# Kernel optimization log

Measured on AMD Instinct MI355X. Metric: run time of the kernel, lower is better.

## Reference

```python
import jax, jax.numpy as jnp
import numpy as np

B, N, L, D = 4, 128, 20, 512


def setup_inputs() -> dict:
    key = jax.random.key(0)
    ks = jax.random.split(key, 8)
    return {
        "f_b": jax.random.normal(ks[0], (B, N, D), jnp.float32),
        "f_w": jax.random.normal(ks[1], (B, L, D), jnp.float32),
        "f_s": jax.random.normal(ks[2], (B, D), jnp.float32),
        "f_m": jax.random.normal(ks[3], (B, N, N, D), jnp.float32),
        "Wq": jax.random.normal(ks[4], (D, D), jnp.float32) / np.sqrt(D).astype(np.float32),
        "bq": jax.random.normal(ks[5], (D,), jnp.float32) * 0.02,
        "Wk": jax.random.normal(ks[6], (D, D), jnp.float32) / np.sqrt(D).astype(np.float32),
        "bk": jax.random.normal(ks[7], (D,), jnp.float32) * 0.02,
    }


def reference(f_b, f_w, f_s, f_m, Wq, bq, Wk, bk):
    d = f_b.shape[-1]
    scale = jnp.asarray(1.0 / np.sqrt(d), f_b.dtype)
    # cross-attention: boundary features attend to word features
    q = f_b @ Wq.T + bq                                   # [B,N,D]
    k = f_w @ Wk.T + bk                                   # [B,L,D]
    attn = jax.nn.softmax(jnp.einsum('bnd,bld->bnl', q, k) * scale, axis=-1)
    f_baq = jnp.einsum('bnl,bld->bnd', attn, f_w)         # [B,N,D]
    # sentence-gated boundary features
    f_bq = f_b * (f_baq + f_s[:, None, :])                # [B,N,D]
    # boundary self-attention
    A_b = jax.nn.softmax(jnp.einsum('bnd,bmd->bnm', f_bq, f_bq) * scale, axis=-1)
    f_bb = jnp.einsum('bnm,bmd->bnd', A_b, f_b)           # [B,N,D]
    # gated moment-map reduction: sum_i A_b[b,i,j] * sigmoid(f_m*f_s)*f_m
    g_m = jax.nn.sigmoid(f_m * f_s[:, None, None, :])     # [B,N,N,D]
    f_bm = jnp.einsum('bij,bijd->bjd', A_b, g_m * f_m)    # [B,N,D]
    return f_bb + f_b + f_bm
```

## Files before the change

### kernel.cpp

```cpp
#include <hip/hip_runtime.h>
#include <hip/hip_bf16.h>

#define Bc 4
#define Nc 128
#define Lc 20
#define Dc 512
#define SCALE 0.04419417382415922f
#define NL2E -1.4426950408889634f

#if __has_builtin(__builtin_amdgcn_exp2f)
#define EXP2(x) __builtin_amdgcn_exp2f(x)
#else
#define EXP2(x) __expf((x) * 0.6931471805599453f)
#endif

typedef float vf4 __attribute__((ext_vector_type(4)));

#if __has_builtin(__builtin_nontemporal_load)
#define NT_LOAD4(p) __builtin_nontemporal_load((const vf4*)(p))
#else
#define NT_LOAD4(p) (*(const vf4*)(p))
#endif

__global__ __launch_bounds__(256)
void proj_gemm(const float* __restrict__ f_b, const float* __restrict__ f_w,
               const float* __restrict__ Wq, const float* __restrict__ bq,
               const float* __restrict__ Wk, const float* __restrict__ bk,
               float* __restrict__ qb, float* __restrict__ kb) {
    const int t  = threadIdx.x;
    const int tc = blockIdx.x, ty = blockIdx.y, kz = blockIdx.z;
    const bool isq = ty < 8;
    if (!isq && kz >= 4) return;
    const int c0    = tc * 64;
    const int r0    = isq ? ty * 64 : (ty - 8) * 64;
    const int nrows = isq ? 512 : 80;
    const int KB    = isq ? 64 : 128;
    const int kbase = isq ? kz * 64 : kz * 128;
    const float* Ain  = isq ? f_b : f_w;
    const float* W    = isq ? Wq : Wk;
    const float* bias = isq ? bq : bk;
    float* C          = isq ? (qb + kz * 512 * Dc) : (kb + kz * 80 * Dc);

    __shared__ __align__(16) float As[16][68];
    __shared__ __align__(16) float Bs[16][68];

    const int srow = t >> 2;
    const int sk4  = (t & 3) * 4;
    const int arow = min(r0 + srow, nrows - 1);
    const int wrow = c0 + srow;

    const int rr = (t >> 4) * 4;
    const int cc = (t & 15) * 4;
    float acc[4][4] = {};

    const float* Aptr = Ain + arow * Dc + kbase + sk4;
    const float* Wptr = W   + wrow * Dc + kbase + sk4;
    float4 ga = *(const float4*)Aptr;
    float4 gb = *(const float4*)Wptr;

    for (int kk0 = 16; kk0 <= KB; kk0 += 16) {
        __syncthreads();
        As[sk4 + 0][srow] = ga.x; As[sk4 + 1][srow] = ga.y;
        As[sk4 + 2][srow] = ga.z; As[sk4 + 3][srow] = ga.w;
        Bs[sk4 + 0][srow] = gb.x; Bs[sk4 + 1][srow] = gb.y;
        Bs[sk4 + 2][srow] = gb.z; Bs[sk4 + 3][srow] = gb.w;
        __syncthreads();
        if (kk0 < KB) {
            ga = *(const float4*)(Aptr + kk0);
            gb = *(const float4*)(Wptr + kk0);
        }
#pragma unroll
        for (int kk = 0; kk < 16; kk++) {
            const float4 av = *(const float4*)&As[kk][rr];
            const float4 bv = *(const float4*)&Bs[kk][cc];
            acc[0][0] = fmaf(av.x, bv.x, acc[0][0]);
            acc[0][1] = fmaf(av.x, bv.y, acc[0][1]);
            acc[0][2] = fmaf(av.x, bv.z, acc[0][2]);
            acc[0][3] = fmaf(av.x, bv.w, acc[0][3]);
            acc[1][0] = fmaf(av.y, bv.x, acc[1][0]);
            acc[1][1] = fmaf(av.y, bv.y, acc[1][1]);
            acc[1][2] = fmaf(av.y, bv.z, acc[1][2]);
            acc[1][3] = fmaf(av.y, bv.w, acc[1][3]);
            acc[2][0] = fmaf(av.z, bv.x, acc[2][0]);
            acc[2][1] = fmaf(av.z, bv.y, acc[2][1]);
            acc[2][2] = fmaf(av.z, bv.z, acc[2][2]);
            acc[2][3] = fmaf(av.z, bv.w, acc[2][3]);
            acc[3][0] = fmaf(av.w, bv.x, acc[3][0]);
            acc[3][1] = fmaf(av.w, bv.y, acc[3][1]);
            acc[3][2] = fmaf(av.w, bv.z, acc[3][2]);
            acc[3][3] = fmaf(av.w, bv.w, acc[3][3]);
        }
    }

    float4 bv4 = make_float4(0.f, 0.f, 0.f, 0.f);
    if (kz == 0) bv4 = *(const float4*)&bias[c0 + cc];
#pragma unroll
    for (int i = 0; i < 4; i++) {
        const int orow = r0 + rr + i;
        if (orow < nrows) {
            float4 o;
            o.x = acc[i][0] + bv4.x; o.y = acc[i][1] + bv4.y;
            o.z = acc[i][2] + bv4.z; o.w = acc[i][3] + bv4.w;
            *(float4*)&C[orow * Dc + c0 + cc] = o;
        }
    }
}

__global__ __launch_bounds__(256)
void cross_attn_gate(const float* __restrict__ qb, const float* __restrict__ kb,
                     const float* __restrict__ f_w, const float* __restrict__ f_b,
                     const float* __restrict__ f_s, float* __restrict__ f_bq) {
    const int bn = blockIdx.x;
    const int b  = bn >> 7;
    const int t  = threadIdx.x;
    const int lane = t & 63, wave = t >> 6;

    __shared__ __align__(16) float qs[Dc];
    __shared__ float sc[32];
    __shared__ float invs;

    {
        float2 s = make_float2(0.f, 0.f);
#pragma unroll
        for (int h = 0; h < 8; h++) {
            const float2 u = ((const float2*)(qb + h * 512 * Dc + bn * Dc))[t];
            s.x += u.x; s.y += u.y;
        }
        ((float2*)qs)[t] = s;
    }
    __syncthreads();

    const float4* q4 = (const float4*)qs;
    const float4 qa = q4[lane];
    const float4 qv = q4[lane + 64];

    for (int l = wave; l < Lc; l += 4) {
        float4 ka = make_float4(0.f, 0.f, 0.f, 0.f);
        float4 kv = make_float4(0.f, 0.f, 0.f, 0.f);
#pragma unroll
        for (int h = 0; h < 4; h++) {
            const float4* kr = (const float4*)(kb + h * 80 * Dc + (b * Lc + l) * Dc);
            const float4 u = kr[lane];
            const float4 v = kr[lane + 64];
            ka.x += u.x; ka.y += u.y; ka.z += u.z; ka.w += u.w;
            kv.x += v.x; kv.y += v.y; kv.z += v.z; kv.w += v.w;
        }
        float s = qa.x * ka.x + qa.y * ka.y + qa.z * ka.z + qa.w * ka.w
                + qv.x * kv.x + qv.y * kv.y + qv.z * kv.z + qv.w * kv.w;
#pragma unroll
        for (int d = 32; d >= 1; d >>= 1) s += __shfl_down(s, d, 64);
        if (lane == 0) sc[l] = s * SCALE;
    }
    __syncthreads();

    if (t == 0) {
        float mx = sc[0];
        for (int l = 1; l < Lc; l++) mx = fmaxf(mx, sc[l]);
        float sum = 0.f;
        for (int l = 0; l < Lc; l++) { float e = __expf(sc[l] - mx); sc[l] = e; sum += e; }
        invs = 1.0f / sum;
    }
    __syncthreads();
    const float inv = invs;

    const float2* fw2 = (const float2*)(f_w + b * Lc * Dc);
    float2 acc = make_float2(0.f, 0.f);
#pragma unroll 5
    for (int l = 0; l < Lc; l++) {
        const float2 v = fw2[l * 256 + t];
        const float w = sc[l];
        acc.x = fmaf(w, v.x, acc.x);
        acc.y = fmaf(w, v.y, acc.y);
    }
    const float2 s2 = ((const float2*)(f_s + b * Dc))[t];
    const float2 fb2 = ((const float2*)(f_b + bn * Dc))[t];
    float2 o;
    o.x = fb2.x * (acc.x * inv + s2.x);
    o.y = fb2.y * (acc.y * inv + s2.y);
    ((float2*)(f_bq + bn * Dc))[t] = o;
}

__global__ __launch_bounds__(512)
void self_attn_scores(const float* __restrict__ f_bq,
                      float* __restrict__ A_b, float* __restrict__ A_bT) {
    const int bn = blockIdx.x;
    const int b  = bn >> 7, n = bn & 127;
    const int t  = threadIdx.x;
    const int lane = t & 63, wave = t >> 6;

    __shared__ __align__(16) float qrow[Dc];
    __shared__ float sc[Nc];
    __shared__ float redm[2];
    __shared__ float reds[2];

    qrow[t] = f_bq[bn * Dc + t];
    __syncthreads();

    const float4* q4 = (const float4*)qrow;
    const float4 qa = q4[lane];
    const float4 qv = q4[lane + 64];

    for (int m = wave; m < Nc; m += 8) {
        const float4* kr = (const float4*)(f_bq + (b * Nc + m) * Dc);
        const float4 va = kr[lane];
        const float4 vb = kr[lane + 64];
        float s = qa.x * va.x + qa.y * va.y + qa.z * va.z + qa.w * va.w
                + qv.x * vb.x + qv.y * vb.y + qv.z * vb.z + qv.w * vb.w;
#pragma unroll
        for (int d = 32; d >= 1; d >>= 1) s += __shfl_down(s, d, 64);
        if (lane == 0) sc[m] = s * SCALE;
    }
    __syncthreads();

    float sval = 0.f, e = 0.f;
    if (t < Nc) {
        sval = sc[t];
        float m = sval;
#pragma unroll
        for (int d = 32; d >= 1; d >>= 1) m = fmaxf(m, __shfl_xor(m, d, 64));
        if (lane == 0) redm[wave] = m;
    }
    __syncthreads();
    if (t < Nc) {
        const float mx = fmaxf(redm[0], redm[1]);
        e = __expf(sval - mx);
        float s = e;
#pragma unroll
        for (int d = 32; d >= 1; d >>= 1) s += __shfl_xor(s, d, 64);
        if (lane == 0) reds[wave] = s;
    }
    __syncthreads();
    if (t < Nc) {
        const float a = e * (1.0f / (reds[0] + reds[1]));
        A_b[bn * Nc + t] = a;
        A_bT[(b * Nc + t) * Nc + n] = a;
    }
}

__global__ __launch_bounds__(256, 4)
void moment_final(const float* __restrict__ f_m, const float* __restrict__ f_s,
                  const float* __restrict__ A_b, const float* __restrict__ A_bT,
                  const float* __restrict__ f_b, float* __restrict__ out) {
    const int bj = blockIdx.x;
    const int b  = bj >> 7, j = bj & 127;
    const int dh = blockIdx.y;
    const int t  = threadIdx.x;
    const int c  = t & 63;
    const int g  = t >> 6;

    __shared__ float w[Nc];
    __shared__ float ar[Nc];
    __shared__ __align__(16) float4 pex[3][64];

    if (t < Nc) w[t] = A_bT[bj * Nc + t];
    else        ar[t - Nc] = A_b[bj * Nc + (t - Nc)];
    __syncthreads();

    const int c4 = dh * 64 + c;
    const float4 s4 = ((const float4*)(f_s + b * Dc))[c4];
    const float4 ns = make_float4(NL2E * s4.x, NL2E * s4.y, NL2E * s4.z, NL2E * s4.w);

    float4 acc = make_float4(0.f, 0.f, 0.f, 0.f);
    const float* fm = f_m;
    const long istride = (long)Nc * Dc;
    long idx = ((long)(b * Nc + g * 32) * Nc + j) * Dc + c4 * 4;

#pragma unroll 1
    for (int ii = 0; ii < 32; ii += 8) {
        vf4 mv[8];
#pragma unroll
        for (int u = 0; u < 8; u++)
            mv[u] = NT_LOAD4(fm + idx + (long)u * istride);
        idx += 8 * istride;
#pragma unroll
        for (int u = 0; u < 8; u++) {
            const float ww = w[g * 32 + ii + u];
            const vf4 m4 = mv[u];
            acc.x = fmaf(ww * m4.x, __builtin_amdgcn_rcpf(1.f + EXP2(m4.x * ns.x)), acc.x);
            acc.y = fmaf(ww * m4.y, __builtin_amdgcn_rcpf(1.f + EXP2(m4.y * ns.y)), acc.y);
            acc.z = fmaf(ww * m4.z, __builtin_amdgcn_rcpf(1.f + EXP2(m4.z * ns.z)), acc.z);
            acc.w = fmaf(ww * m4.w, __builtin_amdgcn_rcpf(1.f + EXP2(m4.w * ns.w)), acc.w);
        }
    }

    const float4* fb4 = (const float4*)(f_b + b * Nc * Dc);
    const int mbase = g * 32;
#pragma unroll 4
    for (int m = mbase; m < mbase + 32; m++) {
        const float a = ar[m];
        const float4 v = fb4[m * (Dc / 4) + c4];
        acc.x = fmaf(a, v.x, acc.x); acc.y = fmaf(a, v.y, acc.y);
        acc.z = fmaf(a, v.z, acc.z); acc.w = fmaf(a, v.w, acc.w);
    }

    if (g != 0) pex[g - 1][c] = acc;
    __syncthreads();
    if (g == 0) {
#pragma unroll
        for (int p = 0; p < 3; p++) {
            const float4 q = pex[p][c];
            acc.x += q.x; acc.y += q.y; acc.z += q.z; acc.w += q.w;
        }
        const float4 r = fb4[j * (Dc / 4) + c4];
        acc.x += r.x; acc.y += r.y; acc.z += r.z; acc.w += r.w;
        ((float4*)out)[bj * (Dc / 4) + c4] = acc;
    }
}

extern "C" void kernel_launch(void* const* d_in, const int* in_sizes, int n_in,
                              void* d_out, int out_size, void* d_ws, size_t ws_size,
                              hipStream_t stream) {
    const float* f_b = (const float*)d_in[0];
    const float* f_w = (const float*)d_in[1];
    const float* f_s = (const float*)d_in[2];
    const float* f_m = (const float*)d_in[3];
    const float* Wq  = (const float*)d_in[4];
    const float* bq  = (const float*)d_in[5];
    const float* Wk  = (const float*)d_in[6];
    const float* bk  = (const float*)d_in[7];
    float* out = (float*)d_out;

    float* ws   = (float*)d_ws;
    float* qb   = ws;
    float* kb   = qb   + 8 * 512 * Dc;
    float* f_bq = kb   + 4 * 80 * Dc;
    float* A_b  = f_bq + 512 * Dc;
    float* A_bT = A_b  + 512 * Nc;

    proj_gemm<<<dim3(8, 10, 8), 256, 0, stream>>>(f_b, f_w, Wq, bq, Wk, bk, qb, kb);
    cross_attn_gate<<<Bc * Nc, 256, 0, stream>>>(qb, kb, f_w, f_b, f_s, f_bq);
    self_attn_scores<<<Bc * Nc, 512, 0, stream>>>(f_bq, A_b, A_bT);
    moment_final<<<dim3(Bc * Nc, 2), 256, 0, stream>>>(f_m, f_s, A_b, A_bT, f_b, out);
}
```

Baseline: 234.1 us.

## Prefetch f_m into cache via extra blocks in earlier kernels

Adds extra blocks to the projection, cross-attention and self-attention kernels that only load slices of the large f_m tensor and discard the values, so the data sits in cache (likely the large last-level cache) before the moment reduction kernel runs. The moment kernel switches from nontemporal loads to normal cached loads so it can hit those lines. The aim is to overlap reading the dominant f_m traffic with the small earlier kernels. The risk is that f_m (128 MB) is larger than the cache, so most of it will be evicted and the extra reads add DRAM traffic.

```diff
diff --git a/kernel.cpp b/kernel.cpp
--- a/kernel.cpp
+++ b/kernel.cpp
@@ -14,25 +14,34 @@
 #define EXP2(x) __expf((x) * 0.6931471805599453f)
 #endif
 
-typedef float vf4 __attribute__((ext_vector_type(4)));
-
-#if __has_builtin(__builtin_nontemporal_load)
-#define NT_LOAD4(p) __builtin_nontemporal_load((const vf4*)(p))
-#else
-#define NT_LOAD4(p) (*(const vf4*)(p))
-#endif
+
+__device__ __forceinline__ void prefetch_fm(const float4* p, int iters, int stride) {
+    for (int it = 0; it < iters; ++it) {
+        const float4 v = p[it * stride];
+        asm volatile("" :: "v"(v.x), "v"(v.y), "v"(v.z), "v"(v.w));
+    }
+}
 
 __global__ __launch_bounds__(256)
 void proj_gemm(const float* __restrict__ f_b, const float* __restrict__ f_w,
                const float* __restrict__ Wq, const float* __restrict__ bq,
                const float* __restrict__ Wk, const float* __restrict__ bk,
+               const float* __restrict__ f_m,
                float* __restrict__ qb, float* __restrict__ kb) {
-    const int t  = threadIdx.x;
-    const int tc = blockIdx.x, ty = blockIdx.y, kz = blockIdx.z;
-    const bool isq = ty < 8;
-    if (!isq && kz >= 4) return;
+    const int bid = blockIdx.x;
+    const int t   = threadIdx.x;
+
+    if (bid >= 576) {
+        prefetch_fm((const float4*)f_m + (long)(bid - 576) * 4096 + t, 16, 256);
+        return;
+    }
+
+    const bool isq = bid < 512;
+    int tc, ty, kz;
+    if (isq) { kz = bid >> 6; ty = (bid >> 3) & 7; tc = bid & 7; }
+    else     { const int x = bid - 512; kz = x >> 4; ty = (x >> 3) & 1; tc = x & 7; }
     const int c0    = tc * 64;
-    const int r0    = isq ? ty * 64 : (ty - 8) * 64;
+    const int r0    = ty * 64;
     const int nrows = isq ? 512 : 80;
     const int KB    = isq ? 64 : 128;
     const int kbase = isq ? kz * 64 : kz * 128;
@@ -109,10 +118,18 @@
 __global__ __launch_bounds__(256)
 void cross_attn_gate(const float* __restrict__ qb, const float* __restrict__ kb,
                      const float* __restrict__ f_w, const float* __restrict__ f_b,
-                     const float* __restrict__ f_s, float* __restrict__ f_bq) {
-    const int bn = blockIdx.x;
+                     const float* __restrict__ f_s, const float* __restrict__ f_m,
+                     float* __restrict__ f_bq) {
+    const int bid = blockIdx.x;
+    const int t  = threadIdx.x;
+
+    if (bid >= 512) {
+        prefetch_fm((const float4*)f_m + 1835008L + (long)(bid - 512) * 4096 + t, 16, 256);
+        return;
+    }
+
+    const int bn = bid;
     const int b  = bn >> 7;
-    const int t  = threadIdx.x;
     const int lane = t & 63, wave = t >> 6;
 
     __shared__ __align__(16) float qs[Dc];
@@ -181,11 +198,18 @@
 }
 
 __global__ __launch_bounds__(512)
-void self_attn_scores(const float* __restrict__ f_bq,
+void self_attn_scores(const float* __restrict__ f_bq, const float* __restrict__ f_m,
                       float* __restrict__ A_b, float* __restrict__ A_bT) {
-    const int bn = blockIdx.x;
+    const int bid = blockIdx.x;
+    const int t  = threadIdx.x;
+
+    if (bid >= 512) {
+        prefetch_fm((const float4*)f_m + 3932160L + (long)(bid - 512) * 5120 + t, 10, 512);
+        return;
+    }
+
+    const int bn = bid;
     const int b  = bn >> 7, n = bn & 127;
-    const int t  = threadIdx.x;
     const int lane = t & 63, wave = t >> 6;
 
     __shared__ __align__(16) float qrow[Dc];
@@ -261,21 +285,21 @@
     const float4 ns = make_float4(NL2E * s4.x, NL2E * s4.y, NL2E * s4.z, NL2E * s4.w);
 
     float4 acc = make_float4(0.f, 0.f, 0.f, 0.f);
-    const float* fm = f_m;
-    const long istride = (long)Nc * Dc;
-    long idx = ((long)(b * Nc + g * 32) * Nc + j) * Dc + c4 * 4;
+    const float4* fm4 = (const float4*)f_m;
+    const long istride = (long)Nc * (Dc / 4);
+    long idx = ((long)(b * Nc + g * 32) * Nc + j) * (Dc / 4) + c4;
 
 #pragma unroll 1
     for (int ii = 0; ii < 32; ii += 8) {
-        vf4 mv[8];
+        float4 mv[8];
 #pragma unroll
         for (int u = 0; u < 8; u++)
-            mv[u] = NT_LOAD4(fm + idx + (long)u * istride);
+            mv[u] = fm4[idx + (long)u * istride];
         idx += 8 * istride;
 #pragma unroll
         for (int u = 0; u < 8; u++) {
             const float ww = w[g * 32 + ii + u];
-            const vf4 m4 = mv[u];
+            const float4 m4 = mv[u];
             acc.x = fmaf(ww * m4.x, __builtin_amdgcn_rcpf(1.f + EXP2(m4.x * ns.x)), acc.x);
             acc.y = fmaf(ww * m4.y, __builtin_amdgcn_rcpf(1.f + EXP2(m4.y * ns.y)), acc.y);
             acc.z = fmaf(ww * m4.z, __builtin_amdgcn_rcpf(1.f + EXP2(m4.z * ns.z)), acc.z);
@@ -327,8 +351,8 @@
     float* A_b  = f_bq + 512 * Dc;
     float* A_bT = A_b  + 512 * Nc;
 
-    proj_gemm<<<dim3(8, 10, 8), 256, 0, stream>>>(f_b, f_w, Wq, bq, Wk, bk, qb, kb);
-    cross_attn_gate<<<Bc * Nc, 256, 0, stream>>>(qb, kb, f_w, f_b, f_s, f_bq);
-    self_attn_scores<<<Bc * Nc, 512, 0, stream>>>(f_bq, A_b, A_bT);
+    proj_gemm<<<1024, 256, 0, stream>>>(f_b, f_w, Wq, bq, Wk, bk, f_m, qb, kb);
+    cross_attn_gate<<<1024, 256, 0, stream>>>(qb, kb, f_w, f_b, f_s, f_m, f_bq);
+    self_attn_scores<<<1024, 512, 0, stream>>>(f_bq, f_m, A_b, A_bT);
     moment_final<<<dim3(Bc * Nc, 2), 256, 0, stream>>>(f_m, f_s, A_b, A_bT, f_b, out);
 }
```

New measurement: 242.3 us. 1.03x slower.
